# Kernel optimization log

Measured on AMD Instinct MI355X. Metric: run time of the kernel, lower is better.

The kernel has to match this reference:

```python
import jax, jax.numpy as jnp
import numpy as np

N_NODES = 50000
N_EDGES = 800000
IN_CH = 512
HID = 256
HEADS = 8
OUT_CH = 64


def _glorot(key, shape):
    fan_in = shape[0] if len(shape) == 2 else shape[-1]
    return jax.random.normal(key, shape, jnp.float32) / jnp.sqrt(jnp.float32(fan_in))


def setup_inputs() -> dict:
    key = jax.random.key(0)
    ks = jax.random.split(key, 16)
    C = HID // HEADS  # 32, per-head dim
    return {
        "x": jax.random.normal(ks[0], (N_NODES, IN_CH), jnp.float32),
        "edge_index": jax.random.randint(ks[1], (2, N_EDGES), 0, N_NODES, jnp.int32),
        # layer 0: in -> heads*C, concat
        "W0": _glorot(ks[2], (IN_CH, HEADS * C)),
        "a_src0": _glorot(ks[3], (HEADS, C)),
        "a_dst0": _glorot(ks[4], (HEADS, C)),
        "b0": jnp.zeros((HEADS * C,), jnp.float32),
        # layer 1: hidden -> heads*C, concat
        "W1": _glorot(ks[5], (HID, HEADS * C)),
        "a_src1": _glorot(ks[6], (HEADS, C)),
        "a_dst1": _glorot(ks[7], (HEADS, C)),
        "b1": jnp.zeros((HEADS * C,), jnp.float32),
        # layer 2: hidden -> out_ch, 1 head, mean (concat=False)
        "W2": _glorot(ks[8], (HID, 1 * OUT_CH)),
        "a_src2": _glorot(ks[9], (1, OUT_CH)),
        "a_dst2": _glorot(ks[10], (1, OUT_CH)),
        "b2": jnp.zeros((OUT_CH,), jnp.float32),
    }


def gat_conv(x, W, a_src, a_dst, b, src, dst, concat):
    """PyG GATConv (self-loops already appended to src/dst), eval mode."""
    N = x.shape[0]
    H, C = a_src.shape
    h = (x @ W).reshape(N, H, C)                      # [N,H,C]
    alpha_src = jnp.sum(h * a_src, axis=-1)           # [N,H]
    alpha_dst = jnp.sum(h * a_dst, axis=-1)           # [N,H]
    e = jax.nn.leaky_relu(alpha_src[src] + alpha_dst[dst], 0.2)  # [E,H]
    # softmax over incoming edges per destination node
    m = jax.ops.segment_max(e, dst, num_segments=N)   # [N,H]
    m = jnp.where(jnp.isfinite(m), m, 0.0)
    w = jnp.exp(e - m[dst])
    s = jax.ops.segment_sum(w, dst, num_segments=N)
    alpha = w / (s[dst] + 1e-16)                      # [E,H]
    out = jax.ops.segment_sum(alpha[:, :, None] * h[src], dst, num_segments=N)
    out = out.reshape(N, H * C) if concat else out.mean(axis=1)
    return out + b


def reference(x, edge_index, W0, a_src0, a_dst0, b0, W1, a_src1, a_dst1, b1, W2, a_src2, a_dst2, b2):
    N = x.shape[0]
    loop = jnp.arange(N, dtype=edge_index.dtype)      # add_self_loops=True
    src = jnp.concatenate([edge_index[0], loop])
    dst = jnp.concatenate([edge_index[1], loop])
    # dropout is identity in eval mode
    h = jax.nn.elu(gat_conv(x, W0, a_src0, a_dst0, b0, src, dst, True))
    h = jax.nn.elu(gat_conv(h, W1, a_src1, a_dst1, b1, src, dst, True))
    h = gat_conv(h, W2, a_src2, a_dst2, b2, src, dst, False)
    return jax.nn.log_softmax(h, axis=1)
```

## Files before the change

### kernel.cpp

```cpp
#include <hip/hip_runtime.h>
#include <hip/hip_bf16.h>

typedef __attribute__((ext_vector_type(8))) short short8;
typedef __attribute__((ext_vector_type(4))) float f32x4;
typedef __attribute__((ext_vector_type(2))) float f32x2;
typedef __attribute__((ext_vector_type(4))) unsigned short us4;

__device__ __forceinline__ ushort f2bf(float f) {
    unsigned u = __float_as_uint(f);
    u += 0x7FFFu + ((u >> 16) & 1u);
    return (ushort)(u >> 16);
}
__device__ __forceinline__ float bf2f(ushort h) {
    return __uint_as_float(((unsigned)h) << 16);
}
__device__ __forceinline__ float lrelu(float e) { return (e >= 0.f) ? e : 0.2f * e; }
__device__ __forceinline__ unsigned char f2fp8(float v) {
    return (unsigned char)(__builtin_amdgcn_cvt_pk_fp8_f32(v, v, 0, false) & 0xFF);
}
__device__ __forceinline__ void gload16(const void* g, void* l) {
    __builtin_amdgcn_global_load_lds(
        (const __attribute__((address_space(1))) unsigned int*)g,
        (__attribute__((address_space(3))) unsigned int*)l, 16, 0, 0);
}

__global__ void k_hist(const int* __restrict__ dst, int* __restrict__ deg, int e) {
    int i = blockIdx.x * blockDim.x + threadIdx.x;
    if (i < e) atomicAdd(&deg[dst[i]], 1);
}
__global__ void k_scanA(const int* __restrict__ deg, int* __restrict__ bsum, int n) {
    __shared__ int sd[256];
    int t = blockIdx.x * 256 + threadIdx.x;
    sd[threadIdx.x] = (t < n) ? deg[t] + 1 : 0;
    __syncthreads();
    for (int off = 128; off > 0; off >>= 1) {
        if (threadIdx.x < off) sd[threadIdx.x] += sd[threadIdx.x + off];
        __syncthreads();
    }
    if (threadIdx.x == 0) bsum[blockIdx.x] = sd[0];
}
__global__ void k_scanC(const int* __restrict__ deg, const int* __restrict__ bsum,
                        int* __restrict__ rowptr, int* __restrict__ cursor,
                        int n, int etot, int nb) {
    __shared__ int sb[256];
    __shared__ int sd[256];
    __shared__ int sbx[256];
    int i = threadIdx.x;
    int bv = (i < nb) ? bsum[i] : 0;
    sb[i] = bv;
    __syncthreads();
    for (int off = 1; off < 256; off <<= 1) {
        int tv = (i >= off) ? sb[i - off] : 0;
        __syncthreads();
        sb[i] += tv;
        __syncthreads();
    }
    sbx[i] = sb[i] - bv;
    __syncthreads();
    int boff = sbx[blockIdx.x];

    int t = blockIdx.x * 256 + i;
    int v = (t < n) ? deg[t] + 1 : 0;
    sd[i] = v;
    __syncthreads();
    for (int off = 1; off < 256; off <<= 1) {
        int tv = (i >= off) ? sd[i - off] : 0;
        __syncthreads();
        sd[i] += tv;
        __syncthreads();
    }
    if (t < n) {
        int ex = boff + sd[i] - v;
        rowptr[t] = ex;
        cursor[t] = ex;
        if (t == n - 1) rowptr[n] = etot;
    }
}
__global__ void k_scatter(const int* __restrict__ ei, int* __restrict__ cursor,
                          int* __restrict__ col, int e, int n) {
    int i = blockIdx.x * blockDim.x + threadIdx.x;
    int etot = e + n;
    if (i >= etot) return;
    int s, d;
    if (i < e) { s = ei[i]; d = ei[e + i]; }
    else       { s = i - e; d = s; }
    int pos = atomicAdd(&cursor[d], 1);
    col[pos] = s;
}

__global__ void k_wcvt3(const float* __restrict__ W0, ushort* __restrict__ T0,
                        const float* __restrict__ W1, ushort* __restrict__ T1,
                        const float* __restrict__ W2, ushort* __restrict__ T2,
                        int* __restrict__ deg, int n) {
    int i = blockIdx.x * blockDim.x + threadIdx.x;
    if (i < n) deg[i] = 0;
    if (i < 131072) {
        int k = i >> 8, c = i & 255;
        T0[(size_t)c * 512 + k] = f2bf(W0[i]);
    } else if (i < 196608) {
        int j = i - 131072;
        int k = j >> 8, c = j & 255;
        T1[(size_t)c * 256 + k] = f2bf(W1[j]);
    } else if (i < 212992) {
        int j = i - 196608;
        int k = j >> 6, c = j & 63;
        T2[(size_t)c * 256 + k] = f2bf(W2[j]);
    }
}

template <int K, int BN, bool AF32>
__global__ __launch_bounds__(256) void k_gemm(const void* __restrict__ Ap,
                                              const ushort* __restrict__ BT,
                                              unsigned char* __restrict__ Cp,
                                              const float* __restrict__ asv,
                                              const float* __restrict__ adv,
                                              float* __restrict__ asrc,
                                              float* __restrict__ adst, int M) {
    constexpr int BM = 64, BK = 32;
    constexpr int NK = K / BK;
    constexpr int NF = BN / 32;
    constexpr int AU = BM * BK / 8;
    constexpr int BU = BN * BK / 8;
    constexpr int TU = AU + BU;
    __shared__ __align__(16) ushort lds[2][TU * 8];

    const int t = threadIdx.x;
    const int wid = t >> 6, lane = t & 63;
    const int lr = lane & 15, lg = lane >> 4;
    const int wm = wid >> 1, wn = wid & 1;
    const int bm0 = blockIdx.x * BM;
    const int bn0 = blockIdx.y * BN;
    const int Nc = BN * gridDim.y;

    int a_off[2], b_off[NF];
#pragma unroll
    for (int mf = 0; mf < 2; ++mf) {
        int row = wm * 32 + mf * 16 + lr;
        a_off[mf] = row * 64 + ((lg ^ ((row >> 1) & 3)) << 4);
    }
#pragma unroll
    for (int nf = 0; nf < NF; ++nf) {
        int col = wn * (BN / 2) + nf * 16 + lr;
        b_off[nf] = AU * 16 + col * 64 + ((lg ^ ((col >> 1) & 3)) << 4);
    }

    f32x4 acc[2][NF];
#pragma unroll
    for (int mf = 0; mf < 2; ++mf)
#pragma unroll
        for (int nf = 0; nf < NF; ++nf) acc[mf][nf] = f32x4{0.f, 0.f, 0.f, 0.f};

    f32x4 ra[2];

    auto stage_B = [&](int buf, int kk) {
#pragma unroll
        for (int i = 0; i < 2; ++i) {
            int u = t + i * 256;
            int col = u >> 2;
            int g = (u & 3) ^ ((col >> 1) & 3);
            const ushort* src = BT + (size_t)(bn0 + col) * K + kk + g * 8;
            gload16(src, &lds[buf][(AU + u) * 8]);
        }
    };
    auto stage_A16 = [&](int buf, int kk) {
        int u = t;
        int row = u >> 2;
        int g = (u & 3) ^ ((row >> 1) & 3);
        int grow = bm0 + row;
        if (grow >= M) grow = M - 1;
        const ushort* src = (const ushort*)Ap + (size_t)grow * K + kk + g * 8;
        gload16(src, &lds[buf][u * 8]);
    };
    auto load_A32 = [&](int kk) {
        int u = t;
        int row = u >> 2;
        int g = (u & 3) ^ ((row >> 1) & 3);
        int grow = bm0 + row;
        if (grow >= M) grow = M - 1;
        const float* src = (const float*)Ap + (size_t)grow * K + kk + g * 8;
        ra[0] = *(const f32x4*)src;
        ra[1] = *(const f32x4*)(src + 4);
    };
    auto write_A32 = [&](int buf) {
        int u = t;
        short8 v;
#pragma unroll
        for (int j = 0; j < 4; ++j) {
            v[j] = (short)f2bf(ra[0][j]);
            v[4 + j] = (short)f2bf(ra[1][j]);
        }
        *(short8*)&lds[buf][u * 8] = v;
    };
    auto compute = [&](int buf) {
        const char* base = (const char*)lds[buf];
        short8 af[2], bf_[NF];
#pragma unroll
        for (int mf = 0; mf < 2; ++mf) af[mf] = *(const short8*)(base + a_off[mf]);
#pragma unroll
        for (int nf = 0; nf < NF; ++nf) bf_[nf] = *(const short8*)(base + b_off[nf]);
#pragma unroll
        for (int mf = 0; mf < 2; ++mf)
#pragma unroll
            for (int nf = 0; nf < NF; ++nf)
                acc[mf][nf] = __builtin_amdgcn_mfma_f32_16x16x32_bf16(af[mf], bf_[nf], acc[mf][nf], 0, 0, 0);
    };

    if constexpr (AF32) {
        load_A32(0);
        write_A32(0);
    } else {
        stage_A16(0, 0);
    }
    stage_B(0, 0);
    __syncthreads();

    int buf = 0;
    for (int ks = 0; ks < NK; ++ks) {
        const int kk = (ks + 1) * BK;
        if (ks + 1 < NK) {
            if constexpr (AF32) load_A32(kk);
            else stage_A16(buf ^ 1, kk);
            stage_B(buf ^ 1, kk);
        }
        compute(buf);
        if constexpr (AF32) {
            if (ks + 1 < NK) write_A32(buf ^ 1);
        }
        __syncthreads();
        buf ^= 1;
    }

#pragma unroll
    for (int mf = 0; mf < 2; ++mf) {
#pragma unroll
        for (int nf = 0; nf < NF; ++nf) {
            int col = bn0 + wn * (BN / 2) + nf * 16 + lr;
#pragma unroll
            for (int p = 0; p < 4; ++p) {
                int row = bm0 + wm * 32 + mf * 16 + lg * 4 + p;
                if (row < M)
                    Cp[(size_t)row * Nc + col] = f2fp8(acc[mf][nf][p]);
            }
        }
    }

    if constexpr (NF == 4) {
        float cs[4], cd[4];
#pragma unroll
        for (int nf = 0; nf < 4; ++nf) {
            int col = bn0 + wn * 64 + nf * 16 + lr;
            cs[nf] = asv[col];
            cd[nf] = adv[col];
        }
        const int hb = (bn0 >> 5) + wn * 2;
#pragma unroll
        for (int mf = 0; mf < 2; ++mf) {
#pragma unroll
            for (int p = 0; p < 4; ++p) {
                float sA = acc[mf][0][p] * cs[0] + acc[mf][1][p] * cs[1];
                float sB = acc[mf][2][p] * cs[2] + acc[mf][3][p] * cs[3];
                float dA = acc[mf][0][p] * cd[0] + acc[mf][1][p] * cd[1];
                float dB = acc[mf][2][p] * cd[2] + acc[mf][3][p] * cd[3];
#pragma unroll
                for (int off = 1; off < 16; off <<= 1) {
                    sA += __shfl_xor(sA, off);
                    sB += __shfl_xor(sB, off);
                    dA += __shfl_xor(dA, off);
                    dB += __shfl_xor(dB, off);
                }
                int row = bm0 + wm * 32 + mf * 16 + lg * 4 + p;
                if (lr == 0 && row < M) {
                    asrc[row * 8 + hb] = sA;
                    asrc[row * 8 + hb + 1] = sB;
                    adst[row * 8 + hb] = dA;
                    adst[row * 8 + hb + 1] = dB;
                }
            }
        }
    }
}

__global__ __launch_bounds__(256) void k_gemm2(const ushort* __restrict__ Ap,
                                               const ushort* __restrict__ BT,
                                               ushort* __restrict__ Cp,
                                               const float* __restrict__ asv,
                                               const float* __restrict__ adv,
                                               float* __restrict__ asrc,
                                               float* __restrict__ adst, int M) {
    constexpr int K = 256, BM = 64, BK = 32;
    constexpr int NK = K / BK;
    constexpr int AU = BM * BK / 8;
    constexpr int BU = 64 * BK / 8;
    constexpr int TU = AU + BU;
    __shared__ __align__(16) ushort lds[2][TU * 8];

    const int t = threadIdx.x;
    const int wid = t >> 6, lane = t & 63;
    const int lr = lane & 15, lg = lane >> 4;
    const int bm0 = blockIdx.x * BM;

    int a_off0, b_off[4];
    {
        int row = wid * 16 + lr;
        a_off0 = row * 64 + ((lg ^ ((row >> 1) & 3)) << 4);
    }
#pragma unroll
    for (int nf = 0; nf < 4; ++nf) {
        int col = nf * 16 + lr;
        b_off[nf] = AU * 16 + col * 64 + ((lg ^ ((col >> 1) & 3)) << 4);
    }

    f32x4 acc[4];
#pragma unroll
    for (int nf = 0; nf < 4; ++nf) acc[nf] = f32x4{0.f, 0.f, 0.f, 0.f};

    auto stage_B = [&](int buf, int kk) {
        int u = t;
        int col = u >> 2;
        int g = (u & 3) ^ ((col >> 1) & 3);
        const ushort* src = BT + (size_t)col * K + kk + g * 8;
        gload16(src, &lds[buf][(AU + u) * 8]);
    };
    auto stage_A = [&](int buf, int kk) {
        int u = t;
        int row = u >> 2;
        int g = (u & 3) ^ ((row >> 1) & 3);
        int grow = bm0 + row;
        if (grow >= M) grow = M - 1;
        const ushort* src = Ap + (size_t)grow * K + kk + g * 8;
        gload16(src, &lds[buf][u * 8]);
    };
    auto compute = [&](int buf) {
        const char* base = (const char*)lds[buf];
        short8 af = *(const short8*)(base + a_off0);
        short8 bf_[4];
#pragma unroll
        for (int nf = 0; nf < 4; ++nf) bf_[nf] = *(const short8*)(base + b_off[nf]);
#pragma unroll
        for (int nf = 0; nf < 4; ++nf)
            acc[nf] = __builtin_amdgcn_mfma_f32_16x16x32_bf16(af, bf_[nf], acc[nf], 0, 0, 0);
    };

    stage_A(0, 0);
    stage_B(0, 0);
    __syncthreads();
    int buf = 0;
    for (int ks = 0; ks < NK; ++ks) {
        if (ks + 1 < NK) {
            stage_A(buf ^ 1, (ks + 1) * BK);
            stage_B(buf ^ 1, (ks + 1) * BK);
        }
        compute(buf);
        __syncthreads();
        buf ^= 1;
    }

    float cs[4], cd[4];
#pragma unroll
    for (int nf = 0; nf < 4; ++nf) {
        cs[nf] = asv[nf * 16 + lr];
        cd[nf] = adv[nf * 16 + lr];
    }
#pragma unroll
    for (int p = 0; p < 4; ++p) {
        int row = bm0 + wid * 16 + lg * 4 + p;
#pragma unroll
        for (int nf = 0; nf < 4; ++nf) {
            if (row < M)
                Cp[(size_t)row * 64 + nf * 16 + lr] = f2bf(acc[nf][p]);
        }
        float sA = acc[0][p] * cs[0] + acc[1][p] * cs[1] +
                   acc[2][p] * cs[2] + acc[3][p] * cs[3];
        float dA = acc[0][p] * cd[0] + acc[1][p] * cd[1] +
                   acc[2][p] * cd[2] + acc[3][p] * cd[3];
#pragma unroll
        for (int off = 1; off < 16; off <<= 1) {
            sA += __shfl_xor(sA, off);
            dA += __shfl_xor(dA, off);
        }
        if (lr == 0 && row < M) {
            asrc[row] = sA;
            adst[row] = dA;
        }
    }
}

#define MAXW 96
__global__ __launch_bounds__(128) void k_agg(const unsigned char* __restrict__ h8,
                                             const float* __restrict__ asrc,
                                             const float* __restrict__ adst,
                                             const int* __restrict__ rowptr,
                                             const int* __restrict__ col,
                                             const float* __restrict__ bias,
                                             ushort* __restrict__ anext, int n) {
    __shared__ float wl[2][MAXW * 8];
    int wid = threadIdx.x >> 6;
    int lane = threadIdx.x & 63;
    int node = blockIdx.x * 2 + wid;
    if (node >= n) return;
    int beg = rowptr[node], end = rowptr[node + 1];
    int deg = end - beg;
    int hd = lane >> 3;
    int eo = lane & 7;
    float ad = adst[node * 8 + hd];
    float* wp = wl[wid];

    float sacc = 0.f;
    for (int jb = eo; jb < deg; jb += 8) {
        int s = col[beg + jb];
        float w = __expf(lrelu(asrc[s * 8 + hd] + ad));
        if (jb < MAXW) wp[jb * 8 + hd] = w;
        sacc += w;
    }
    sacc += __shfl_xor(sacc, 1);
    sacc += __shfl_xor(sacc, 2);
    sacc += __shfl_xor(sacc, 4);
    float inv = 1.f / (sacc + 1e-16f);

    int nl = (deg < MAXW) ? deg : MAXW;
    float a0 = 0.f, a1 = 0.f, a2 = 0.f, a3 = 0.f;
    int jb = 0;
    for (; jb + 8 <= nl; jb += 8) {
        int sv[8];
#pragma unroll
        for (int i = 0; i < 8; ++i) sv[i] = col[beg + jb + i];
        unsigned gv[8];
#pragma unroll
        for (int i = 0; i < 8; ++i) gv[i] = *(const unsigned*)(h8 + (size_t)sv[i] * 256 + lane * 4);
        float wv[8];
#pragma unroll
        for (int i = 0; i < 8; ++i) wv[i] = wp[(jb + i) * 8 + hd];
#pragma unroll
        for (int i = 0; i < 8; ++i) {
            a0 += wv[i] * __builtin_amdgcn_cvt_f32_fp8(gv[i], 0);
            a1 += wv[i] * __builtin_amdgcn_cvt_f32_fp8(gv[i], 1);
            a2 += wv[i] * __builtin_amdgcn_cvt_f32_fp8(gv[i], 2);
            a3 += wv[i] * __builtin_amdgcn_cvt_f32_fp8(gv[i], 3);
        }
    }
    for (; jb < nl; ++jb) {
        int s = col[beg + jb];
        unsigned g = *(const unsigned*)(h8 + (size_t)s * 256 + lane * 4);
        float w = wp[jb * 8 + hd];
        a0 += w * __builtin_amdgcn_cvt_f32_fp8(g, 0);
        a1 += w * __builtin_amdgcn_cvt_f32_fp8(g, 1);
        a2 += w * __builtin_amdgcn_cvt_f32_fp8(g, 2);
        a3 += w * __builtin_amdgcn_cvt_f32_fp8(g, 3);
    }
    for (; jb < deg; ++jb) {
        int s = col[beg + jb];
        unsigned g = *(const unsigned*)(h8 + (size_t)s * 256 + lane * 4);
        float w = __expf(lrelu(asrc[s * 8 + hd] + ad));
        a0 += w * __builtin_amdgcn_cvt_f32_fp8(g, 0);
        a1 += w * __builtin_amdgcn_cvt_f32_fp8(g, 1);
        a2 += w * __builtin_amdgcn_cvt_f32_fp8(g, 2);
        a3 += w * __builtin_amdgcn_cvt_f32_fp8(g, 3);
    }
    f32x4 bv = *(const f32x4*)(bias + lane * 4);
    float v0 = a0 * inv + bv[0];
    float v1 = a1 * inv + bv[1];
    float v2 = a2 * inv + bv[2];
    float v3 = a3 * inv + bv[3];
    v0 = (v0 > 0.f) ? v0 : expm1f(v0);
    v1 = (v1 > 0.f) ? v1 : expm1f(v1);
    v2 = (v2 > 0.f) ? v2 : expm1f(v2);
    v3 = (v3 > 0.f) ? v3 : expm1f(v3);
    us4 o;
    o[0] = f2bf(v0); o[1] = f2bf(v1); o[2] = f2bf(v2); o[3] = f2bf(v3);
    *(us4*)(anext + (size_t)node * 256 + lane * 4) = o;
}

__global__ __launch_bounds__(128) void k_agg2(const ushort* __restrict__ h2,
                                              const float* __restrict__ asrc,
                                              const float* __restrict__ adst,
                                              const int* __restrict__ rowptr,
                                              const int* __restrict__ col,
                                              const float* __restrict__ bias,
                                              float* __restrict__ out, int n) {
    int wid = threadIdx.x >> 6;
    int lane = threadIdx.x & 63;
    int node = blockIdx.x * 2 + wid;
    if (node >= n) return;
    int beg = rowptr[node], end = rowptr[node + 1];
    int deg = end - beg;
    float ad = adst[node];
    int g = lane >> 3;
    int ch = (lane & 7) * 8;

    f32x2 acc2[4];
#pragma unroll
    for (int i = 0; i < 4; ++i) acc2[i] = f32x2{0.f, 0.f};
    float ssum = 0.f;
    for (int p = 0; p < deg; p += 8) {
        int jb = p + g;
        float w = 0.f;
        uint4 gv = {0u, 0u, 0u, 0u};
        if (jb < deg) {
            int s = col[beg + jb];
            gv = *(const uint4*)(h2 + (size_t)s * 64 + ch);
            w = __expf(lrelu(asrc[s] + ad));
        }
        ssum += w;
        f32x2 w2 = {w, w};
        f32x2 p0 = {__uint_as_float(gv.x << 16), __uint_as_float(gv.x & 0xFFFF0000u)};
        f32x2 p1 = {__uint_as_float(gv.y << 16), __uint_as_float(gv.y & 0xFFFF0000u)};
        f32x2 p2 = {__uint_as_float(gv.z << 16), __uint_as_float(gv.z & 0xFFFF0000u)};
        f32x2 p3 = {__uint_as_float(gv.w << 16), __uint_as_float(gv.w & 0xFFFF0000u)};
        acc2[0] += w2 * p0;
        acc2[1] += w2 * p1;
        acc2[2] += w2 * p2;
        acc2[3] += w2 * p3;
    }
    float v[8];
#pragma unroll
    for (int i = 0; i < 4; ++i) { v[2 * i] = acc2[i].x; v[2 * i + 1] = acc2[i].y; }
#pragma unroll
    for (int off = 8; off < 64; off <<= 1) {
        ssum += __shfl_xor(ssum, off);
#pragma unroll
        for (int i = 0; i < 8; ++i) v[i] += __shfl_xor(v[i], off);
    }
    float inv = 1.f / (ssum + 1e-16f);
#pragma unroll
    for (int i = 0; i < 8; ++i) v[i] = v[i] * inv + bias[ch + i];
    float mx = v[0];
#pragma unroll
    for (int i = 1; i < 8; ++i) mx = fmaxf(mx, v[i]);
    mx = fmaxf(mx, __shfl_xor(mx, 1));
    mx = fmaxf(mx, __shfl_xor(mx, 2));
    mx = fmaxf(mx, __shfl_xor(mx, 4));
    float se = 0.f;
#pragma unroll
    for (int i = 0; i < 8; ++i) se += __expf(v[i] - mx);
    se += __shfl_xor(se, 1);
    se += __shfl_xor(se, 2);
    se += __shfl_xor(se, 4);
    float ls = mx + logf(se);
    if (g == 0) {
        f32x4 o0, o1;
#pragma unroll
        for (int i = 0; i < 4; ++i) { o0[i] = v[i] - ls; o1[i] = v[4 + i] - ls; }
        *(f32x4*)(out + (size_t)node * 64 + ch) = o0;
        *(f32x4*)(out + (size_t)node * 64 + ch + 4) = o1;
    }
}

extern "C" void kernel_launch(void* const* d_in, const int* in_sizes, int n_in,
                              void* d_out, int out_size, void* d_ws, size_t ws_size,
                              hipStream_t stream) {
    const float* x   = (const float*)d_in[0];
    const int*   ei  = (const int*)d_in[1];
    const float* W0  = (const float*)d_in[2];
    const float* as0 = (const float*)d_in[3];
    const float* ad0 = (const float*)d_in[4];
    const float* b0  = (const float*)d_in[5];
    const float* W1  = (const float*)d_in[6];
    const float* as1 = (const float*)d_in[7];
    const float* ad1 = (const float*)d_in[8];
    const float* b1  = (const float*)d_in[9];
    const float* W2  = (const float*)d_in[10];
    const float* as2 = (const float*)d_in[11];
    const float* ad2 = (const float*)d_in[12];
    const float* b2  = (const float*)d_in[13];
    float* out = (float*)d_out;

    const int N = in_sizes[0] / 512;
    const int E = in_sizes[1] / 2;
    const int ETOT = E + N;

    char* ws = (char*)d_ws;
    size_t off = 0;
    auto alloc = [&](size_t bytes) -> void* {
        off = (off + 255) & ~(size_t)255;
        void* p = ws + off;
        off += bytes;
        return p;
    };
    int* rowptr = (int*)alloc((size_t)(N + 1) * 4);
    int* cursor = (int*)alloc((size_t)N * 4);
    int* deg    = (int*)alloc((size_t)N * 4);
    int* bsum   = (int*)alloc(1024);
    int* colb   = (int*)alloc((size_t)ETOT * 4);
    ushort* WT0 = (ushort*)alloc((size_t)256 * 512 * 2);
    ushort* WT1 = (ushort*)alloc((size_t)256 * 256 * 2);
    ushort* WT2 = (ushort*)alloc((size_t)64 * 256 * 2);
    unsigned char* h8 = (unsigned char*)alloc((size_t)N * 256);
    ushort* abf = (ushort*)alloc((size_t)N * 256 * 2);
    float* asrc = (float*)alloc((size_t)N * 8 * 4);
    float* adst = (float*)alloc((size_t)N * 8 * 4);
    ushort* h2   = (ushort*)h8;
    float* asrc2 = asrc;
    float* adst2 = adst;

    const int nblk = (N + 255) / 256;

    k_wcvt3<<<832, 256, 0, stream>>>(W0, WT0, W1, WT1, W2, WT2, deg, N);

    k_hist<<<(E + 255) / 256, 256, 0, stream>>>(ei + E, deg, E);
    k_scanA<<<nblk, 256, 0, stream>>>(deg, bsum, N);
    k_scanC<<<nblk, 256, 0, stream>>>(deg, bsum, rowptr, cursor, N, ETOT, nblk);
    k_scatter<<<(ETOT + 255) / 256, 256, 0, stream>>>(ei, cursor, colb, E, N);

    const dim3 g01((N + 63) / 64, 2);
    const int gblk = (N + 63) / 64;
    const int ablk = (N + 1) / 2;

    k_gemm<512, 128, true><<<g01, 256, 0, stream>>>(x, WT0, h8, as0, ad0, asrc, adst, N);
    k_agg<<<ablk, 128, 0, stream>>>(h8, asrc, adst, rowptr, colb, b0, abf, N);

    k_gemm<256, 128, false><<<g01, 256, 0, stream>>>(abf, WT1, h8, as1, ad1, asrc, adst, N);
    k_agg<<<ablk, 128, 0, stream>>>(h8, asrc, adst, rowptr, colb, b1, abf, N);

    k_gemm2<<<gblk, 256, 0, stream>>>(abf, WT2, h2, as2, ad2, asrc2, adst2, N);
    k_agg2<<<ablk, 128, 0, stream>>>(h2, asrc2, adst2, rowptr, colb, b2, out, N);
}
```

Baseline: 324.9 us.

## Load GEMM A operand directly into registers and give each wave a full-width row strip

The A tile is no longer staged through LDS. Each lane reads its MFMA A fragment straight from global memory into registers, converting from fp32 in-register for the first layer, and prefetches one K-step ahead. The wave layout also changes from a 2x2 split to four 16-row strips spanning all 128 columns, so each wave now holds 8 accumulators. This cuts LDS traffic and the LDS write plus conversion step, at the cost of uncoalesced global reads of A (each lane fetches 16 or 32 bytes from a different row) and more accumulator registers.

```diff
diff --git a/kernel.cpp b/kernel.cpp
--- a/kernel.cpp
+++ b/kernel.cpp
@@ -22,6 +22,15 @@
     __builtin_amdgcn_global_load_lds(
         (const __attribute__((address_space(1))) unsigned int*)g,
         (__attribute__((address_space(3))) unsigned int*)l, 16, 0, 0);
+}
+__device__ __forceinline__ short8 cvt8(f32x4 a, f32x4 b) {
+    short8 v;
+#pragma unroll
+    for (int j = 0; j < 4; ++j) {
+        v[j] = (short)f2bf(a[j]);
+        v[4 + j] = (short)f2bf(b[j]);
+    }
+    return v;
 }
 
 __global__ void k_hist(const int* __restrict__ dst, int* __restrict__ deg, int e) {
@@ -108,7 +117,7 @@
     }
 }
 
-template <int K, int BN, bool AF32>
+template <int K, bool AF32>
 __global__ __launch_bounds__(256) void k_gemm(const void* __restrict__ Ap,
                                               const ushort* __restrict__ BT,
                                               unsigned char* __restrict__ Cp,
@@ -116,41 +125,33 @@
                                               const float* __restrict__ adv,
                                               float* __restrict__ asrc,
                                               float* __restrict__ adst, int M) {
-    constexpr int BM = 64, BK = 32;
+    constexpr int BM = 64, BK = 32, BN = 128;
     constexpr int NK = K / BK;
-    constexpr int NF = BN / 32;
-    constexpr int AU = BM * BK / 8;
     constexpr int BU = BN * BK / 8;
-    constexpr int TU = AU + BU;
-    __shared__ __align__(16) ushort lds[2][TU * 8];
+    __shared__ __align__(16) ushort lds[2][BU * 8];
 
     const int t = threadIdx.x;
     const int wid = t >> 6, lane = t & 63;
     const int lr = lane & 15, lg = lane >> 4;
-    const int wm = wid >> 1, wn = wid & 1;
     const int bm0 = blockIdx.x * BM;
     const int bn0 = blockIdx.y * BN;
-    const int Nc = BN * gridDim.y;
-
-    int a_off[2], b_off[NF];
-#pragma unroll
-    for (int mf = 0; mf < 2; ++mf) {
-        int row = wm * 32 + mf * 16 + lr;
-        a_off[mf] = row * 64 + ((lg ^ ((row >> 1) & 3)) << 4);
-    }
-#pragma unroll
-    for (int nf = 0; nf < NF; ++nf) {
-        int col = wn * (BN / 2) + nf * 16 + lr;
-        b_off[nf] = AU * 16 + col * 64 + ((lg ^ ((col >> 1) & 3)) << 4);
-    }
-
-    f32x4 acc[2][NF];
-#pragma unroll
-    for (int mf = 0; mf < 2; ++mf)
-#pragma unroll
-        for (int nf = 0; nf < NF; ++nf) acc[mf][nf] = f32x4{0.f, 0.f, 0.f, 0.f};
-
-    f32x4 ra[2];
+
+    int arow = bm0 + wid * 16 + lr;
+    if (arow >= M) arow = M - 1;
+
+    int b_off[8];
+#pragma unroll
+    for (int nf = 0; nf < 8; ++nf) {
+        int col = nf * 16 + lr;
+        b_off[nf] = col * 64 + ((lg ^ ((col >> 1) & 3)) << 4);
+    }
+
+    f32x4 acc[8];
+#pragma unroll
+    for (int nf = 0; nf < 8; ++nf) acc[nf] = f32x4{0.f, 0.f, 0.f, 0.f};
+
+    f32x4 rn0, rn1;
+    short8 aNext;
 
     auto stage_B = [&](int buf, int kk) {
 #pragma unroll
@@ -159,121 +160,88 @@
             int col = u >> 2;
             int g = (u & 3) ^ ((col >> 1) & 3);
             const ushort* src = BT + (size_t)(bn0 + col) * K + kk + g * 8;
-            gload16(src, &lds[buf][(AU + u) * 8]);
-        }
-    };
-    auto stage_A16 = [&](int buf, int kk) {
-        int u = t;
-        int row = u >> 2;
-        int g = (u & 3) ^ ((row >> 1) & 3);
-        int grow = bm0 + row;
-        if (grow >= M) grow = M - 1;
-        const ushort* src = (const ushort*)Ap + (size_t)grow * K + kk + g * 8;
-        gload16(src, &lds[buf][u * 8]);
-    };
-    auto load_A32 = [&](int kk) {
-        int u = t;
-        int row = u >> 2;
-        int g = (u & 3) ^ ((row >> 1) & 3);
-        int grow = bm0 + row;
-        if (grow >= M) grow = M - 1;
-        const float* src = (const float*)Ap + (size_t)grow * K + kk + g * 8;
-        ra[0] = *(const f32x4*)src;
-        ra[1] = *(const f32x4*)(src + 4);
-    };
-    auto write_A32 = [&](int buf) {
-        int u = t;
-        short8 v;
-#pragma unroll
-        for (int j = 0; j < 4; ++j) {
-            v[j] = (short)f2bf(ra[0][j]);
-            v[4 + j] = (short)f2bf(ra[1][j]);
-        }
-        *(short8*)&lds[buf][u * 8] = v;
-    };
-    auto compute = [&](int buf) {
+            gload16(src, &lds[buf][u * 8]);
+        }
+    };
+    auto load_A = [&](int kk) {
+        if constexpr (AF32) {
+            const float* src = (const float*)Ap + (size_t)arow * K + kk + lg * 8;
+            rn0 = *(const f32x4*)src;
+            rn1 = *(const f32x4*)(src + 4);
+        } else {
+            aNext = *(const short8*)((const ushort*)Ap + (size_t)arow * K + kk + lg * 8);
+        }
+    };
+    auto compute = [&](int buf, short8 af) {
         const char* base = (const char*)lds[buf];
-        short8 af[2], bf_[NF];
-#pragma unroll
-        for (int mf = 0; mf < 2; ++mf) af[mf] = *(const short8*)(base + a_off[mf]);
-#pragma unroll
-        for (int nf = 0; nf < NF; ++nf) bf_[nf] = *(const short8*)(base + b_off[nf]);
-#pragma unroll
-        for (int mf = 0; mf < 2; ++mf)
-#pragma unroll
-            for (int nf = 0; nf < NF; ++nf)
-                acc[mf][nf] = __builtin_amdgcn_mfma_f32_16x16x32_bf16(af[mf], bf_[nf], acc[mf][nf], 0, 0, 0);
-    };
-
-    if constexpr (AF32) {
-        load_A32(0);
-        write_A32(0);
-    } else {
-        stage_A16(0, 0);
-    }
+        short8 bf_[8];
+#pragma unroll
+        for (int nf = 0; nf < 8; ++nf) bf_[nf] = *(const short8*)(base + b_off[nf]);
+#pragma unroll
+        for (int nf = 0; nf < 8; ++nf)
+            acc[nf] = __builtin_amdgcn_mfma_f32_16x16x32_bf16(af, bf_[nf], acc[nf], 0, 0, 0);
+    };
+
+    load_A(0);
     stage_B(0, 0);
     __syncthreads();
 
     int buf = 0;
     for (int ks = 0; ks < NK; ++ks) {
-        const int kk = (ks + 1) * BK;
+        short8 aCur;
+        if constexpr (AF32) aCur = cvt8(rn0, rn1);
+        else aCur = aNext;
         if (ks + 1 < NK) {
-            if constexpr (AF32) load_A32(kk);
-            else stage_A16(buf ^ 1, kk);
-            stage_B(buf ^ 1, kk);
-        }
-        compute(buf);
-        if constexpr (AF32) {
-            if (ks + 1 < NK) write_A32(buf ^ 1);
-        }
+            load_A((ks + 1) * BK);
+            stage_B(buf ^ 1, (ks + 1) * BK);
+        }
+        compute(buf, aCur);
         __syncthreads();
         buf ^= 1;
     }
 
 #pragma unroll
-    for (int mf = 0; mf < 2; ++mf) {
-#pragma unroll
-        for (int nf = 0; nf < NF; ++nf) {
-            int col = bn0 + wn * (BN / 2) + nf * 16 + lr;
-#pragma unroll
-            for (int p = 0; p < 4; ++p) {
-                int row = bm0 + wm * 32 + mf * 16 + lg * 4 + p;
-                if (row < M)
-                    Cp[(size_t)row * Nc + col] = f2fp8(acc[mf][nf][p]);
-            }
-        }
-    }
-
-    if constexpr (NF == 4) {
-        float cs[4], cd[4];
-#pragma unroll
-        for (int nf = 0; nf < 4; ++nf) {
-            int col = bn0 + wn * 64 + nf * 16 + lr;
+    for (int nf = 0; nf < 8; ++nf) {
+        int col = bn0 + nf * 16 + lr;
+#pragma unroll
+        for (int p = 0; p < 4; ++p) {
+            int row = bm0 + wid * 16 + lg * 4 + p;
+            if (row < M)
+                Cp[(size_t)row * 256 + col] = f2fp8(acc[nf][p]);
+        }
+    }
+
+    {
+        float cs[8], cd[8];
+#pragma unroll
+        for (int nf = 0; nf < 8; ++nf) {
+            int col = bn0 + nf * 16 + lr;
             cs[nf] = asv[col];
             cd[nf] = adv[col];
         }
-        const int hb = (bn0 >> 5) + wn * 2;
-#pragma unroll
-        for (int mf = 0; mf < 2; ++mf) {
-#pragma unroll
-            for (int p = 0; p < 4; ++p) {
-                float sA = acc[mf][0][p] * cs[0] + acc[mf][1][p] * cs[1];
-                float sB = acc[mf][2][p] * cs[2] + acc[mf][3][p] * cs[3];
-                float dA = acc[mf][0][p] * cd[0] + acc[mf][1][p] * cd[1];
-                float dB = acc[mf][2][p] * cd[2] + acc[mf][3][p] * cd[3];
-#pragma unroll
-                for (int off = 1; off < 16; off <<= 1) {
-                    sA += __shfl_xor(sA, off);
-                    sB += __shfl_xor(sB, off);
-                    dA += __shfl_xor(dA, off);
-                    dB += __shfl_xor(dB, off);
+        const int hb = bn0 >> 5;
+#pragma unroll
+        for (int p = 0; p < 4; ++p) {
+            float s[4], d[4];
+#pragma unroll
+            for (int hh = 0; hh < 4; ++hh) {
+                s[hh] = acc[2 * hh][p] * cs[2 * hh] + acc[2 * hh + 1][p] * cs[2 * hh + 1];
+                d[hh] = acc[2 * hh][p] * cd[2 * hh] + acc[2 * hh + 1][p] * cd[2 * hh + 1];
+            }
+#pragma unroll
+            for (int off = 1; off < 16; off <<= 1) {
+#pragma unroll
+                for (int hh = 0; hh < 4; ++hh) {
+                    s[hh] += __shfl_xor(s[hh], off);
+                    d[hh] += __shfl_xor(d[hh], off);
                 }
-                int row = bm0 + wm * 32 + mf * 16 + lg * 4 + p;
-                if (lr == 0 && row < M) {
-                    asrc[row * 8 + hb] = sA;
-                    asrc[row * 8 + hb + 1] = sB;
-                    adst[row * 8 + hb] = dA;
-                    adst[row * 8 + hb + 1] = dB;
+            }
+            int row = bm0 + wid * 16 + lg * 4 + p;
+            if (lr == 0 && row < M) {
+#pragma unroll
+                for (int hh = 0; hh < 4; ++hh) {
+                    asrc[row * 8 + hb + hh] = s[hh];
+                    adst[row * 8 + hb + hh] = d[hh];
                 }
             }
         }
@@ -289,50 +257,41 @@
                                                float* __restrict__ adst, int M) {
     constexpr int K = 256, BM = 64, BK = 32;
     constexpr int NK = K / BK;
-    constexpr int AU = BM * BK / 8;
     constexpr int BU = 64 * BK / 8;
-    constexpr int TU = AU + BU;
-    __shared__ __align__(16) ushort lds[2][TU * 8];
+    __shared__ __align__(16) ushort lds[2][BU * 8];
 
     const int t = threadIdx.x;
     const int wid = t >> 6, lane = t & 63;
     const int lr = lane & 15, lg = lane >> 4;
     const int bm0 = blockIdx.x * BM;
 
-    int a_off0, b_off[4];
-    {
-        int row = wid * 16 + lr;
-        a_off0 = row * 64 + ((lg ^ ((row >> 1) & 3)) << 4);
-    }
+    int arow = bm0 + wid * 16 + lr;
+    if (arow >= M) arow = M - 1;
+
+    int b_off[4];
 #pragma unroll
     for (int nf = 0; nf < 4; ++nf) {
         int col = nf * 16 + lr;
-        b_off[nf] = AU * 16 + col * 64 + ((lg ^ ((col >> 1) & 3)) << 4);
+        b_off[nf] = col * 64 + ((lg ^ ((col >> 1) & 3)) << 4);
     }
 
     f32x4 acc[4];
 #pragma unroll
     for (int nf = 0; nf < 4; ++nf) acc[nf] = f32x4{0.f, 0.f, 0.f, 0.f};
 
+    short8 aNext;
     auto stage_B = [&](int buf, int kk) {
         int u = t;
         int col = u >> 2;
         int g = (u & 3) ^ ((col >> 1) & 3);
         const ushort* src = BT + (size_t)col * K + kk + g * 8;
-        gload16(src, &lds[buf][(AU + u) * 8]);
-    };
-    auto stage_A = [&](int buf, int kk) {
-        int u = t;
-        int row = u >> 2;
-        int g = (u & 3) ^ ((row >> 1) & 3);
-        int grow = bm0 + row;
-        if (grow >= M) grow = M - 1;
-        const ushort* src = Ap + (size_t)grow * K + kk + g * 8;
         gload16(src, &lds[buf][u * 8]);
     };
-    auto compute = [&](int buf) {
+    auto load_A = [&](int kk) {
+        aNext = *(const short8*)(Ap + (size_t)arow * K + kk + lg * 8);
+    };
+    auto compute = [&](int buf, short8 af) {
         const char* base = (const char*)lds[buf];
-        short8 af = *(const short8*)(base + a_off0);
         short8 bf_[4];
 #pragma unroll
         for (int nf = 0; nf < 4; ++nf) bf_[nf] = *(const short8*)(base + b_off[nf]);
@@ -341,16 +300,17 @@
             acc[nf] = __builtin_amdgcn_mfma_f32_16x16x32_bf16(af, bf_[nf], acc[nf], 0, 0, 0);
     };
 
-    stage_A(0, 0);
+    load_A(0);
     stage_B(0, 0);
     __syncthreads();
     int buf = 0;
     for (int ks = 0; ks < NK; ++ks) {
+        short8 aCur = aNext;
         if (ks + 1 < NK) {
-            stage_A(buf ^ 1, (ks + 1) * BK);
+            load_A((ks + 1) * BK);
             stage_B(buf ^ 1, (ks + 1) * BK);
         }
-        compute(buf);
+        compute(buf, aCur);
         __syncthreads();
         buf ^= 1;
     }
@@ -605,10 +565,10 @@
     const int gblk = (N + 63) / 64;
     const int ablk = (N + 1) / 2;
 
-    k_gemm<512, 128, true><<<g01, 256, 0, stream>>>(x, WT0, h8, as0, ad0, asrc, adst, N);
+    k_gemm<512, true><<<g01, 256, 0, stream>>>(x, WT0, h8, as0, ad0, asrc, adst, N);
     k_agg<<<ablk, 128, 0, stream>>>(h8, asrc, adst, rowptr, colb, b0, abf, N);
 
-    k_gemm<256, 128, false><<<g01, 256, 0, stream>>>(abf, WT1, h8, as1, ad1, asrc, adst, N);
+    k_gemm<256, false><<<g01, 256, 0, stream>>>(abf, WT1, h8, as1, ad1, asrc, adst, N);
     k_agg<<<ablk, 128, 0, stream>>>(h8, asrc, adst, rowptr, colb, b1, abf, N);
 
     k_gemm2<<<gblk, 256, 0, stream>>>(abf, WT2, h2, as2, ad2, asrc2, adst2, N);
```

After: 332.1 us. 2.2% more time.
